# Kernel tuning notes

Hardware: AMD Instinct MI355X
Metric: run time of the kernel (lower is better)

The kernel has to match this reference:

```python
import jax, jax.numpy as jnp
import numpy as np

# ---- config ----
N = 500000
C = 32            # output_coordinate_dim
RES = [256, 256, 256, 64]
J = 2             # wavelet levels
BOUNDS = 1.3
# plane i -> (H, W) of stored plane, and (q, r) coord indices into [x,y,z,t]
# grid_sample convention: coord0 indexes W, coord1 indexes H
PLANE_RES = [(256, 256), (256, 256), (256, 64), (256, 256), (256, 64), (256, 64)]
COORD_IDX = [(0, 1), (0, 2), (3, 0), (1, 2), (3, 1), (3, 2)]

# coif4 decomposition low-pass filter (pywt), 24 taps
DEC_LO = np.array([
    -1.7849850030882614e-06, -3.2596802368833675e-06, 3.1229875865345646e-05,
    6.233903446100713e-05, -0.00025997455248771324, -0.0005890207562443383,
    0.0012665619292989445, 0.003751436157278457, -0.00565828668661072,
    -0.015211731527946259, 0.025082261844864097, 0.03933442712333749,
    -0.09622044203398798, -0.06662747426342504, 0.4343860564914685,
    0.782238930920499, 0.41530840703043026, -0.05607731331675481,
    -0.08126669968087875, 0.026682300156053072, 0.016068943964776348,
    -0.0073461663276420935, -0.0016294920126017326, 0.0008923136685823146],
    dtype=np.float32)
REC_LO = DEC_LO[::-1].copy()                                    # synthesis low-pass
REC_HI = (DEC_LO * ((-1.0) ** np.arange(DEC_LO.shape[0]))).astype(np.float32)  # QMF high-pass


def _up2(x, axis):
    """Insert zeros between samples along axis (upsample by 2)."""
    x = jnp.moveaxis(x, axis, -1)
    z = jnp.zeros(x.shape[:-1] + (2 * x.shape[-1],), x.dtype)
    z = z.at[..., ::2].set(x)
    return jnp.moveaxis(z, -1, axis)


def _circ_conv(x, f, axis):
    """Circular convolution along axis with a short fixed filter (periodization mode)."""
    out = f[0] * x
    for k in range(1, len(f)):
        out = out + f[k] * jnp.roll(x, k, axis=axis)
    return out


def _sfb1d(lo, hi, axis):
    """1D synthesis filter bank: upsample, filter, add. Length L -> 2L."""
    return _circ_conv(_up2(lo, axis), REC_LO, axis) + _circ_conv(_up2(hi, axis), REC_HI, axis)


def _sfb_level(ll, yh):
    """One inverse-DWT level. ll: [1,C,h,w], yh: [1,C,3,h,w] -> [1,C,2h,2w]."""
    lh, hl, hh = yh[:, :, 0], yh[:, :, 1], yh[:, :, 2]
    lo = _sfb1d(ll, lh, axis=2)   # combine along H
    hi = _sfb1d(hl, hh, axis=2)
    return _sfb1d(lo, hi, axis=3)  # combine along W


def _idwt2(yl, yhb, yha):
    """2-level inverse DWT (coif4, periodization). yl coarsest, yhb coarse detail, yha fine detail."""
    x = _sfb_level(yl, yhb)   # H/4 -> H/2
    x = _sfb_level(x, yha)    # H/2 -> H
    return x                  # [1, C, H, W]


def _bilinear_sample(plane, coords):
    """torch.grid_sample(bilinear, align_corners=True) equivalent.
    plane: [C,H,W]; coords: [N,2] in [-1,1], coords[:,0]->W, coords[:,1]->H. Returns [N,C]."""
    Cc, H, W = plane.shape
    x = jnp.clip((coords[:, 0] + 1.0) * 0.5 * (W - 1), 0.0, W - 1.0)
    y = jnp.clip((coords[:, 1] + 1.0) * 0.5 * (H - 1), 0.0, H - 1.0)
    x0 = jnp.clip(jnp.floor(x), 0.0, W - 2.0)
    y0 = jnp.clip(jnp.floor(y), 0.0, H - 2.0)
    wx = x - x0
    wy = y - y0
    x0i = x0.astype(jnp.int32); x1i = x0i + 1
    y0i = y0.astype(jnp.int32); y1i = y0i + 1
    v = (plane[:, y0i, x0i] * (1 - wy) * (1 - wx)
         + plane[:, y0i, x1i] * (1 - wy) * wx
         + plane[:, y1i, x0i] * wy * (1 - wx)
         + plane[:, y1i, x1i] * wy * wx)  # [C,N]
    return v.T


def setup_inputs() -> dict:
    key = jax.random.key(0)
    keys = jax.random.split(key, 2 + 6 * 3)
    inp = {}
    inp["pts"] = jax.random.uniform(keys[0], (N, 3), jnp.float32, -BOUNDS, BOUNDS)
    inp["timestamps"] = jax.random.uniform(keys[1], (N, 1), jnp.float32, 0.0, 1.0)
    for i, (H, W) in enumerate(PLANE_RES):
        k0, k1, k2 = keys[2 + 3 * i], keys[2 + 3 * i + 1], keys[2 + 3 * i + 2]
        # wavelet-domain learned parameters: yl coarsest approx, yha fine detail, yhb coarse detail
        inp[f"yl{i}"] = 0.3 + 0.1 * jax.random.normal(k0, (1, C, H // 4, W // 4), jnp.float32)
        inp[f"yha{i}"] = 0.05 * jax.random.normal(k1, (1, C, 3, H // 2, W // 2), jnp.float32)
        inp[f"yhb{i}"] = 0.05 * jax.random.normal(k2, (1, C, 3, H // 4, W // 4), jnp.float32)
    return inp


def reference(pts, timestamps,
              yl0, yha0, yhb0, yl1, yha1, yhb1, yl2, yha2, yhb2,
              yl3, yha3, yhb3, yl4, yha4, yhb4, yl5, yha5, yhb5):
    coefs = [(yl0, yha0, yhb0), (yl1, yha1, yhb1), (yl2, yha2, yhb2),
             (yl3, yha3, yhb3), (yl4, yha4, yhb4), (yl5, yha5, yhb5)]
    # normalize_aabb with aabb = [[B,B,B],[-B,-B,-B]]
    pts_n = (pts - BOUNDS) * (2.0 / (-2.0 * BOUNDS)) - 1.0
    t = timestamps * 2.0 - 1.0
    p4 = jnp.concatenate([pts_n, t], axis=-1)  # [N,4] = (x,y,z,t) in [-1,1]
    interp = jnp.ones((), jnp.float32)
    for (yl, yha, yhb), (q, r) in zip(coefs, COORD_IDX):
        plane = _idwt2(yl, yhb, yha)[0]                      # [C,H,W] IDWT reconstruction
        coords = jnp.stack([p4[:, q], p4[:, r]], axis=-1)    # [N,2]
        feat = _bilinear_sample(plane, coords)               # [N,C] gather
        interp = interp * feat                               # multiplicative fusion
    return interp
```

## Files before the change

### kernel.cpp

```cpp
#include <hip/hip_runtime.h>
#include <hip/hip_fp16.h>

#define NBIN 4096
#define NREP 8
#define SCAP 32
#define OVCAP 65536
#define BPB 4

__device__ __constant__ float DEC_LO[24] = {
    -1.7849850030882614e-06f, -3.2596802368833675e-06f, 3.1229875865345646e-05f,
    6.233903446100713e-05f, -0.00025997455248771324f, -0.0005890207562443383f,
    0.0012665619292989445f, 0.003751436157278457f, -0.00565828668661072f,
    -0.015211731527946259f, 0.025082261844864097f, 0.03933442712333749f,
    -0.09622044203398798f, -0.06662747426342504f, 0.4343860564914685f,
    0.782238930920499f, 0.41530840703043026f, -0.05607731331675481f,
    -0.08126669968087875f, 0.026682300156053072f, 0.016068943964776348f,
    -0.0073461663276420935f, -0.0016294920126017326f, 0.0008923136685823146f
};

struct PK {
    const float* yl[6];
    const float* yhb[6];
    const float* yha[6];
    float* x1[6];
    __half* lo2[6];
    __half* hi2[6];
    __half* planeH[6];
    const float* pts;
    const float* ts;
    int* cnt;
    int* cum;
    float4* binP4;
    int* binIdx;
    float4* ovP4;
    int* ovIdx;
    int Npts;
};

__device__ __forceinline__ void compute_p4(const float* pts, const float* ts, int p, float* p4) {
    const float sc = (float)(2.0 / (-2.0 * 1.3));
    p4[0] = (pts[p * 3 + 0] - 1.3f) * sc - 1.0f;
    p4[1] = (pts[p * 3 + 1] - 1.3f) * sc - 1.0f;
    p4[2] = (pts[p * 3 + 2] - 1.3f) * sc - 1.0f;
    p4[3] = ts[p] * 2.0f - 1.0f;
}

__device__ __forceinline__ int morton_key(const float* p4) {
    int key = 0;
#pragma unroll
    for (int d = 0; d < 4; ++d) {
        float u = (p4[d] + 1.0f) * 0.5f * 8.0f;
        int ci = (int)u;
        ci = ci < 0 ? 0 : (ci > 7 ? 7 : ci);
#pragma unroll
        for (int b = 0; b < 3; ++b) key |= ((ci >> b) & 1) << (b * 4 + d);
    }
    return key;
}

__global__ __launch_bounds__(256) void k1_l1_zero(PK a) {
    __shared__ struct { float lo[32 * 64], hi[32 * 64]; } sm;
    int bid = blockIdx.x, tid = threadIdx.x;

    if (bid < 768) {
        int rg = bid & 3, c = (bid >> 2) & 31, i = bid >> 7;
        int w4 = (i == 0 || i == 1 || i == 3) ? 64 : 16;
        int lw4 = (w4 == 64) ? 6 : 4;

        const float* llc = a.yl[i] + (size_t)c * 64 * w4;
        const float* lhc = a.yhb[i] + (size_t)(c * 3 + 0) * 64 * w4;
        const float* hlc = a.yhb[i] + (size_t)(c * 3 + 1) * 64 * w4;
        const float* hhc = a.yhb[i] + (size_t)(c * 3 + 2) * 64 * w4;

        for (int idx = tid; idx < (16 << lw4); idx += 256) {
            int mp = idx >> lw4, x = idx & (w4 - 1);
            int m = rg * 16 + mp;
            float lo0 = 0.f, lo1 = 0.f, hi0 = 0.f, hi1 = 0.f;
#pragma unroll
            for (int j = 0; j < 12; ++j) {
                int r = (m - j) & 63;
                int ii = (r << lw4) + x;
                float vll = llc[ii], vlh = lhc[ii], vhl = hlc[ii], vhh = hhc[ii];
                float rl0 = DEC_LO[23 - 2 * j], rl1 = DEC_LO[22 - 2 * j];
                float rh0 = DEC_LO[2 * j],      rh1 = -DEC_LO[2 * j + 1];
                lo0 += rl0 * vll + rh0 * vlh;
                lo1 += rl1 * vll + rh1 * vlh;
                hi0 += rl0 * vhl + rh0 * vhh;
                hi1 += rl1 * vhl + rh1 * vhh;
            }
            sm.lo[((2 * mp) << lw4) + x] = lo0;
            sm.lo[((2 * mp + 1) << lw4) + x] = lo1;
            sm.hi[((2 * mp) << lw4) + x] = hi0;
            sm.hi[((2 * mp + 1) << lw4) + x] = hi1;
        }
        __syncthreads();

        int w2 = w4 * 2;
        float* x1p = a.x1[i] + (size_t)c * 128 * w2;
        for (int idx = tid; idx < (32 << lw4); idx += 256) {
            int yl = idx >> lw4, mcol = idx & (w4 - 1);
            float o0 = 0.f, o1 = 0.f;
#pragma unroll
            for (int j = 0; j < 12; ++j) {
                int r = (mcol - j) & (w4 - 1);
                float vl = sm.lo[(yl << lw4) + r], vh = sm.hi[(yl << lw4) + r];
                o0 += DEC_LO[23 - 2 * j] * vl + DEC_LO[2 * j] * vh;
                o1 += DEC_LO[22 - 2 * j] * vl - DEC_LO[2 * j + 1] * vh;
            }
            *(float2*)(x1p + (size_t)(rg * 32 + yl) * w2 + 2 * mcol) = make_float2(o0, o1);
        }
    } else {
        int idx = (bid - 768) * 256 + tid;
        if (idx <= NREP * NBIN) a.cnt[idx] = 0;
    }
}

__global__ __launch_bounds__(256) void k2_v2_scatter(PK a) {
    int bid = blockIdx.x, tid = threadIdx.x;

    if (bid < 512) {
        const int S = 512 * 256;
        int rep = bid & 7;
        int t = bid * 256 + tid;
        for (int base = 0; base < a.Npts; base += 4 * S) {
            float4 q[4];
            int key[4], pi[4], pos[4];
#pragma unroll
            for (int k = 0; k < 4; ++k) {
                int p = base + t + k * S;
                pi[k] = p;
                if (p < a.Npts) {
                    float p4[4];
                    compute_p4(a.pts, a.ts, p, p4);
                    key[k] = morton_key(p4);
                    q[k] = make_float4(p4[0], p4[1], p4[2], p4[3]);
                } else {
                    key[k] = -1;
                }
            }
#pragma unroll
            for (int k = 0; k < 4; ++k)
                if (key[k] >= 0) pos[k] = atomicAdd(&a.cnt[rep * NBIN + key[k]], 1);
#pragma unroll
            for (int k = 0; k < 4; ++k) {
                if (key[k] < 0) continue;
                if (pos[k] < SCAP) {
                    size_t slot = ((size_t)rep * NBIN + key[k]) * SCAP + pos[k];
                    a.binP4[slot] = q[k];
                    a.binIdx[slot] = pi[k];
                } else {
                    int ov = atomicAdd(&a.cnt[NREP * NBIN], 1);
                    if (ov < OVCAP) {
                        a.ovP4[ov] = q[k];
                        a.ovIdx[ov] = pi[k];
                    }
                }
            }
        }
    } else {
        int ib = bid - 512;
        ib = (ib & 7) * 240 + (ib >> 3);

        const int boff[7] = {0, 512, 1024, 1152, 1664, 1792, 1920};
        int i = 0;
        while (i < 5 && ib >= boff[i + 1]) ++i;
        int lw2 = (i == 0 || i == 1 || i == 3) ? 7 : 5;
        int w2 = 1 << lw2;
        unsigned t = (unsigned)(ib - boff[i]) * 256u + tid;
        unsigned tpc = 32u << lw2;
        unsigned c = t >> (5 + lw2);
        unsigned rem = t & (tpc - 1);
        unsigned m = rem >> (lw2 - 2);
        unsigned x = (rem & (unsigned)((w2 >> 2) - 1)) * 4;
        unsigned hw = 128u << lw2;

        const float* llc = a.x1[i] + (size_t)c * hw;
        const float* lhc = a.yha[i] + (size_t)(c * 3 + 0) * hw;
        const float* hlc = a.yha[i] + (size_t)(c * 3 + 1) * hw;
        const float* hhc = a.yha[i] + (size_t)(c * 3 + 2) * hw;

        float4 acl0 = {0,0,0,0}, acl1 = {0,0,0,0}, ach0 = {0,0,0,0}, ach1 = {0,0,0,0};
#pragma unroll
        for (int j = 0; j < 12; ++j) {
            int r = ((int)m - j) & 127;
            unsigned idx = ((unsigned)r << lw2) + x;
            float4 vll = *(const float4*)(llc + idx);
            float4 vlh = *(const float4*)(lhc + idx);
            float4 vhl = *(const float4*)(hlc + idx);
            float4 vhh = *(const float4*)(hhc + idx);
            float rl0 = DEC_LO[23 - 2 * j], rl1 = DEC_LO[22 - 2 * j];
            float rh0 = DEC_LO[2 * j],      rh1 = -DEC_LO[2 * j + 1];
            acl0.x += rl0 * vll.x + rh0 * vlh.x;  acl0.y += rl0 * vll.y + rh0 * vlh.y;
            acl0.z += rl0 * vll.z + rh0 * vlh.z;  acl0.w += rl0 * vll.w + rh0 * vlh.w;
            acl1.x += rl1 * vll.x + rh1 * vlh.x;  acl1.y += rl1 * vll.y + rh1 * vlh.y;
            acl1.z += rl1 * vll.z + rh1 * vlh.z;  acl1.w += rl1 * vll.w + rh1 * vlh.w;
            ach0.x += rl0 * vhl.x + rh0 * vhh.x;  ach0.y += rl0 * vhl.y + rh0 * vhh.y;
            ach0.z += rl0 * vhl.z + rh0 * vhh.z;  ach0.w += rl0 * vhl.w + rh0 * vhh.w;
            ach1.x += rl1 * vhl.x + rh1 * vhh.x;  ach1.y += rl1 * vhl.y + rh1 * vhh.y;
            ach1.z += rl1 * vhl.z + rh1 * vhh.z;  ach1.w += rl1 * vhl.w + rh1 * vhh.w;
        }
        size_t ob = ((size_t)c * 256 + 2 * m) * w2 + x;
        __half* lp = a.lo2[i] + ob;
        *(__half2*)(lp)          = __floats2half2_rn(acl0.x, acl0.y);
        *(__half2*)(lp + 2)      = __floats2half2_rn(acl0.z, acl0.w);
        *(__half2*)(lp + w2)     = __floats2half2_rn(acl1.x, acl1.y);
        *(__half2*)(lp + w2 + 2) = __floats2half2_rn(acl1.z, acl1.w);
        __half* hpp = a.hi2[i] + ob;
        *(__half2*)(hpp)          = __floats2half2_rn(ach0.x, ach0.y);
        *(__half2*)(hpp + 2)      = __floats2half2_rn(ach0.z, ach0.w);
        *(__half2*)(hpp + w2)     = __floats2half2_rn(ach1.x, ach1.y);
        *(__half2*)(hpp + w2 + 2) = __floats2half2_rn(ach1.z, ach1.w);
    }
}

__global__ __launch_bounds__(256) void k3_ht(PK a) {
    __shared__ struct { __half lo[32 * 130], hi[32 * 130]; } sm;
    int bid = blockIdx.x, tid = threadIdx.x;

    if (bid < 1536) {
        int i = bid >> 8, y = bid & 255;
        int lw2 = (i == 0 || i == 1 || i == 3) ? 7 : 5;
        int w2 = 1 << lw2;
        int stride = w2 + 2;

        for (int idx = tid; idx < (32 << lw2); idx += 256) {
            int c = idx >> lw2, x = idx & (w2 - 1);
            size_t g = ((size_t)c * 256 + y) * w2 + x;
            sm.lo[c * stride + x] = a.lo2[i][g];
            sm.hi[c * stride + x] = a.hi2[i][g];
        }
        __syncthreads();

        int W = 2 * w2;
        __half* orow = a.planeH[i] + (size_t)y * W * 32;
        for (int idx = tid; idx < (32 << lw2); idx += 256) {
            int m = idx >> 5, c = idx & 31;
            float o0 = 0.f, o1 = 0.f;
#pragma unroll
            for (int j = 0; j < 12; ++j) {
                int r2 = m - j; if (r2 < 0) r2 += w2;
                float vl = __half2float(sm.lo[c * stride + r2]);
                float vh = __half2float(sm.hi[c * stride + r2]);
                o0 += DEC_LO[23 - 2 * j] * vl + DEC_LO[2 * j] * vh;
                o1 += DEC_LO[22 - 2 * j] * vl - DEC_LO[2 * j + 1] * vh;
            }
            orow[(2 * m) * 32 + c] = __float2half(o0);
            orow[(2 * m + 1) * 32 + c] = __float2half(o1);
        }
    } else {
        int bin = (bid - 1536) * 256 + tid;
        int c = 0;
#pragma unroll
        for (int r = 0; r < NREP; ++r) {
            int v = a.cnt[r * NBIN + bin];
            c += (v < SCAP ? v : SCAP);
            a.cum[bin * 8 + r] = c;
        }
    }
}

union H8 { float4 f4; __half h[8]; };

struct SK {
    const __half* pl[6];
    const float4* binP4;
    const int* binIdx;
    const int* cnt;
    const int* cum;
    const float4* ovP4;
    const int* ovIdx;
    float* out;
};

__device__ __forceinline__ void sample_pair(const SK& a,
        const float* p4A, int oA, int chA,
        const float* p4B, int oB, int chB, bool hasB) {
    const int PW[6] = {256, 256, 64, 256, 64, 64};
    const int QI[6] = {0, 0, 3, 1, 3, 3};
    const int RI[6] = {1, 2, 0, 2, 1, 2};
    float accA[8] = {1.f, 1.f, 1.f, 1.f, 1.f, 1.f, 1.f, 1.f};
    float accB[8] = {1.f, 1.f, 1.f, 1.f, 1.f, 1.f, 1.f, 1.f};
#pragma unroll
    for (int i = 0; i < 6; ++i) {
        int W = PW[i];
        float fxA = fminf(fmaxf((p4A[QI[i]] + 1.0f) * 0.5f * (float)(W - 1), 0.0f), (float)(W - 1));
        float fyA = fminf(fmaxf((p4A[RI[i]] + 1.0f) * 0.5f * 255.0f, 0.0f), 255.0f);
        float x0A = fminf(floorf(fxA), (float)(W - 2));
        float y0A = fminf(floorf(fyA), 254.0f);
        float wxA = fxA - x0A, wyA = fyA - y0A;
        const __half* baseA = a.pl[i] + ((size_t)(int)y0A * W + (int)x0A) * 32 + chA;
        float fxB = fminf(fmaxf((p4B[QI[i]] + 1.0f) * 0.5f * (float)(W - 1), 0.0f), (float)(W - 1));
        float fyB = fminf(fmaxf((p4B[RI[i]] + 1.0f) * 0.5f * 255.0f, 0.0f), 255.0f);
        float x0B = fminf(floorf(fxB), (float)(W - 2));
        float y0B = fminf(floorf(fyB), 254.0f);
        float wxB = fxB - x0B, wyB = fyB - y0B;
        const __half* baseB = a.pl[i] + ((size_t)(int)y0B * W + (int)x0B) * 32 + chB;

        H8 a00, a01, a10, a11, b00, b01, b10, b11;
        a00.f4 = *(const float4*)(baseA);
        a01.f4 = *(const float4*)(baseA + 32);
        a10.f4 = *(const float4*)(baseA + (size_t)W * 32);
        a11.f4 = *(const float4*)(baseA + (size_t)W * 32 + 32);
        b00.f4 = *(const float4*)(baseB);
        b01.f4 = *(const float4*)(baseB + 32);
        b10.f4 = *(const float4*)(baseB + (size_t)W * 32);
        b11.f4 = *(const float4*)(baseB + (size_t)W * 32 + 32);

        float wA00 = (1.f - wyA) * (1.f - wxA), wA01 = (1.f - wyA) * wxA;
        float wA10 = wyA * (1.f - wxA), wA11 = wyA * wxA;
        float wB00 = (1.f - wyB) * (1.f - wxB), wB01 = (1.f - wyB) * wxB;
        float wB10 = wyB * (1.f - wxB), wB11 = wyB * wxB;
#pragma unroll
        for (int k = 0; k < 8; ++k) {
            accA[k] *= wA00 * __half2float(a00.h[k]) + wA01 * __half2float(a01.h[k]) +
                       wA10 * __half2float(a10.h[k]) + wA11 * __half2float(a11.h[k]);
            accB[k] *= wB00 * __half2float(b00.h[k]) + wB01 * __half2float(b01.h[k]) +
                       wB10 * __half2float(b10.h[k]) + wB11 * __half2float(b11.h[k]);
        }
    }
    float* opA = a.out + (size_t)oA * 32 + chA;
    *(float4*)(opA)     = make_float4(accA[0], accA[1], accA[2], accA[3]);
    *(float4*)(opA + 4) = make_float4(accA[4], accA[5], accA[6], accA[7]);
    if (hasB) {
        float* opB = a.out + (size_t)oB * 32 + chB;
        *(float4*)(opB)     = make_float4(accB[0], accB[1], accB[2], accB[3]);
        *(float4*)(opB + 4) = make_float4(accB[4], accB[5], accB[6], accB[7]);
    }
}

__global__ __launch_bounds__(256) void k4_sample(SK a) {
    int bid = blockIdx.x, tid = threadIdx.x;
    if (bid < NBIN / BPB) {
        int xcd = bid & 7, g = bid >> 3;
        int binBase = xcd * (NBIN / 8) + g * BPB;

#pragma unroll
        for (int bb = 0; bb < BPB; ++bb) {
            int bin = binBase + bb;
            int4 u0 = *(const int4*)(a.cum + bin * 8);
            int4 u1 = *(const int4*)(a.cum + bin * 8 + 4);
            int cums[8] = {u0.x, u0.y, u0.z, u0.w, u1.x, u1.y, u1.z, u1.w};
            int n4 = cums[7] * 4;

            for (int l0 = tid; l0 < n4; l0 += 512) {
                int l1 = l0 + 256;
                bool hasB = l1 < n4;
                int lB = hasB ? l1 : l0;

                int sA = l0 >> 2, chA = (l0 & 3) << 3;
                int sB = lB >> 2, chB = (lB & 3) << 3;
                int rA = 0, bsA = 0, rB = 0, bsB = 0;
#pragma unroll
                for (int rr = 0; rr < NREP - 1; ++rr) {
                    if (sA >= cums[rr]) { rA = rr + 1; bsA = cums[rr]; }
                    if (sB >= cums[rr]) { rB = rr + 1; bsB = cums[rr]; }
                }
                size_t slotA = ((size_t)rA * NBIN + bin) * SCAP + (sA - bsA);
                size_t slotB = ((size_t)rB * NBIN + bin) * SCAP + (sB - bsB);
                float4 qA = a.binP4[slotA];
                float4 qB = a.binP4[slotB];
                int oA = a.binIdx[slotA];
                int oB = a.binIdx[slotB];
                float p4A[4] = {qA.x, qA.y, qA.z, qA.w};
                float p4B[4] = {qB.x, qB.y, qB.z, qB.w};
                sample_pair(a, p4A, oA, chA, p4B, oB, chB, hasB);
            }
        }
    } else {
        int ov = a.cnt[NREP * NBIN];
        ov = ov < OVCAP ? ov : OVCAP;
        int ov4 = ov * 4;
        for (int l0 = (bid - NBIN / BPB) * 256 + tid; l0 < ov4; l0 += 4096) {
            int l1 = l0 + 2048;
            bool hasB = l1 < ov4;
            int lB = hasB ? l1 : l0;
            int sA = l0 >> 2, chA = (l0 & 3) << 3;
            int sB = lB >> 2, chB = (lB & 3) << 3;
            float4 qA = a.ovP4[sA];
            float4 qB = a.ovP4[sB];
            float p4A[4] = {qA.x, qA.y, qA.z, qA.w};
            float p4B[4] = {qB.x, qB.y, qB.z, qB.w};
            sample_pair(a, p4A, a.ovIdx[sA], chA, p4B, a.ovIdx[sB], chB, hasB);
        }
    }
}

extern "C" void kernel_launch(void* const* d_in, const int* in_sizes, int n_in,
                              void* d_out, int out_size, void* d_ws, size_t ws_size,
                              hipStream_t stream) {
    const int PWt[6] = {256, 256, 64, 256, 64, 64};
    const int Npts = in_sizes[0] / 3;

    char* ws = (char*)d_ws;
    PK a;
    size_t off = 0;
    for (int i = 0; i < 6; ++i) {
        int W = PWt[i], w2 = W / 2;
        a.x1[i] = (float*)(ws + off);      off += (size_t)32 * 128 * w2 * 4;
        a.lo2[i] = (__half*)(ws + off);    off += (size_t)32 * 256 * w2 * 2;
        a.hi2[i] = (__half*)(ws + off);    off += (size_t)32 * 256 * w2 * 2;
        a.planeH[i] = (__half*)(ws + off); off += (size_t)256 * W * 32 * 2;
    }
    off = (off + 15) & ~(size_t)15;
    a.binP4 = (float4*)(ws + off);  off += (size_t)NREP * NBIN * SCAP * 16;
    a.ovP4 = (float4*)(ws + off);   off += (size_t)OVCAP * 16;
    a.binIdx = (int*)(ws + off);    off += (size_t)NREP * NBIN * SCAP * 4;
    a.ovIdx = (int*)(ws + off);     off += (size_t)OVCAP * 4;
    a.cnt = (int*)(ws + off);       off += ((size_t)NREP * NBIN + 1) * 4;
    off = (off + 15) & ~(size_t)15;
    a.cum = (int*)(ws + off);       off += (size_t)NBIN * 8 * 4;

    a.pts = (const float*)d_in[0];
    a.ts = (const float*)d_in[1];
    for (int i = 0; i < 6; ++i) {
        a.yl[i] = (const float*)d_in[2 + 3 * i];
        a.yha[i] = (const float*)d_in[3 + 3 * i];
        a.yhb[i] = (const float*)d_in[4 + 3 * i];
    }
    a.Npts = Npts;

    k1_l1_zero<<<768 + 129, 256, 0, stream>>>(a);
    k2_v2_scatter<<<512 + 1920, 256, 0, stream>>>(a);
    k3_ht<<<1536 + 16, 256, 0, stream>>>(a);

    SK s;
    for (int i = 0; i < 6; ++i) s.pl[i] = a.planeH[i];
    s.binP4 = a.binP4; s.binIdx = a.binIdx; s.cnt = a.cnt; s.cum = a.cum;
    s.ovP4 = a.ovP4; s.ovIdx = a.ovIdx;
    s.out = (float*)d_out;
    k4_sample<<<NBIN / BPB + 8, 256, 0, stream>>>(s);
}
```

Before: 249.7 us.

## Split planes into two 16-channel halves and map channel halves to XCDs

Stores each reconstructed plane as two channel-half planes ([2][H][W][16]) instead of interleaved 32 channels. The sampling kernel then assigns each block a single channel half and a bin subset, chosen by the low bits of the block id, so each XCD's L2 only caches one half-plane and a spatial slice of the bins. Each thread processes one point at a time instead of pairs, which cuts per-XCD cache footprint and register pressure. The cost is twice as many blocks and less memory-level parallelism per thread.

```diff
diff --git a/kernel.cpp b/kernel.cpp
--- a/kernel.cpp
+++ b/kernel.cpp
@@ -5,7 +5,6 @@
 #define NREP 8
 #define SCAP 32
 #define OVCAP 65536
-#define BPB 4
 
 __device__ __constant__ float DEC_LO[24] = {
     -1.7849850030882614e-06f, -3.2596802368833675e-06f, 3.1229875865345646e-05f,
@@ -232,7 +231,6 @@
         __syncthreads();
 
         int W = 2 * w2;
-        __half* orow = a.planeH[i] + (size_t)y * W * 32;
         for (int idx = tid; idx < (32 << lw2); idx += 256) {
             int m = idx >> 5, c = idx & 31;
             float o0 = 0.f, o1 = 0.f;
@@ -244,8 +242,10 @@
                 o0 += DEC_LO[23 - 2 * j] * vl + DEC_LO[2 * j] * vh;
                 o1 += DEC_LO[22 - 2 * j] * vl - DEC_LO[2 * j + 1] * vh;
             }
-            orow[(2 * m) * 32 + c] = __float2half(o0);
-            orow[(2 * m + 1) * 32 + c] = __float2half(o1);
+            size_t off = (size_t)(c >> 4) * 256 * W * 16
+                       + ((size_t)y * W + 2 * m) * 16 + (c & 15);
+            a.planeH[i][off] = __float2half(o0);
+            a.planeH[i][off + 16] = __float2half(o1);
         }
     } else {
         int bin = (bid - 1536) * 256 + tid;
@@ -272,115 +272,82 @@
     float* out;
 };
 
-__device__ __forceinline__ void sample_pair(const SK& a,
-        const float* p4A, int oA, int chA,
-        const float* p4B, int oB, int chB, bool hasB) {
+__device__ __forceinline__ void sample8p(const SK& a, const float* p4, int oidx, int c2, int sub) {
     const int PW[6] = {256, 256, 64, 256, 64, 64};
     const int QI[6] = {0, 0, 3, 1, 3, 3};
     const int RI[6] = {1, 2, 0, 2, 1, 2};
-    float accA[8] = {1.f, 1.f, 1.f, 1.f, 1.f, 1.f, 1.f, 1.f};
-    float accB[8] = {1.f, 1.f, 1.f, 1.f, 1.f, 1.f, 1.f, 1.f};
+    float acc[8] = {1.f, 1.f, 1.f, 1.f, 1.f, 1.f, 1.f, 1.f};
 #pragma unroll
     for (int i = 0; i < 6; ++i) {
         int W = PW[i];
-        float fxA = fminf(fmaxf((p4A[QI[i]] + 1.0f) * 0.5f * (float)(W - 1), 0.0f), (float)(W - 1));
-        float fyA = fminf(fmaxf((p4A[RI[i]] + 1.0f) * 0.5f * 255.0f, 0.0f), 255.0f);
-        float x0A = fminf(floorf(fxA), (float)(W - 2));
-        float y0A = fminf(floorf(fyA), 254.0f);
-        float wxA = fxA - x0A, wyA = fyA - y0A;
-        const __half* baseA = a.pl[i] + ((size_t)(int)y0A * W + (int)x0A) * 32 + chA;
-        float fxB = fminf(fmaxf((p4B[QI[i]] + 1.0f) * 0.5f * (float)(W - 1), 0.0f), (float)(W - 1));
-        float fyB = fminf(fmaxf((p4B[RI[i]] + 1.0f) * 0.5f * 255.0f, 0.0f), 255.0f);
-        float x0B = fminf(floorf(fxB), (float)(W - 2));
-        float y0B = fminf(floorf(fyB), 254.0f);
-        float wxB = fxB - x0B, wyB = fyB - y0B;
-        const __half* baseB = a.pl[i] + ((size_t)(int)y0B * W + (int)x0B) * 32 + chB;
-
-        H8 a00, a01, a10, a11, b00, b01, b10, b11;
-        a00.f4 = *(const float4*)(baseA);
-        a01.f4 = *(const float4*)(baseA + 32);
-        a10.f4 = *(const float4*)(baseA + (size_t)W * 32);
-        a11.f4 = *(const float4*)(baseA + (size_t)W * 32 + 32);
-        b00.f4 = *(const float4*)(baseB);
-        b01.f4 = *(const float4*)(baseB + 32);
-        b10.f4 = *(const float4*)(baseB + (size_t)W * 32);
-        b11.f4 = *(const float4*)(baseB + (size_t)W * 32 + 32);
-
-        float wA00 = (1.f - wyA) * (1.f - wxA), wA01 = (1.f - wyA) * wxA;
-        float wA10 = wyA * (1.f - wxA), wA11 = wyA * wxA;
-        float wB00 = (1.f - wyB) * (1.f - wxB), wB01 = (1.f - wyB) * wxB;
-        float wB10 = wyB * (1.f - wxB), wB11 = wyB * wxB;
+        float fx = fminf(fmaxf((p4[QI[i]] + 1.0f) * 0.5f * (float)(W - 1), 0.0f), (float)(W - 1));
+        float fy = fminf(fmaxf((p4[RI[i]] + 1.0f) * 0.5f * 255.0f, 0.0f), 255.0f);
+        float x0 = fminf(floorf(fx), (float)(W - 2));
+        float y0 = fminf(floorf(fy), 254.0f);
+        float wx = fx - x0, wy = fy - y0;
+        int xi = (int)x0, yi = (int)y0;
+
+        const __half* base = a.pl[i] + ((((size_t)c2 * 256 + yi) * W + xi) << 4) + sub * 8;
+        H8 u00, u01, u10, u11;
+        u00.f4 = *(const float4*)(base);
+        u01.f4 = *(const float4*)(base + 16);
+        u10.f4 = *(const float4*)(base + (size_t)W * 16);
+        u11.f4 = *(const float4*)(base + (size_t)W * 16 + 16);
+
+        float w00 = (1.f - wy) * (1.f - wx), w01 = (1.f - wy) * wx;
+        float w10 = wy * (1.f - wx), w11 = wy * wx;
 #pragma unroll
         for (int k = 0; k < 8; ++k) {
-            accA[k] *= wA00 * __half2float(a00.h[k]) + wA01 * __half2float(a01.h[k]) +
-                       wA10 * __half2float(a10.h[k]) + wA11 * __half2float(a11.h[k]);
-            accB[k] *= wB00 * __half2float(b00.h[k]) + wB01 * __half2float(b01.h[k]) +
-                       wB10 * __half2float(b10.h[k]) + wB11 * __half2float(b11.h[k]);
-        }
-    }
-    float* opA = a.out + (size_t)oA * 32 + chA;
-    *(float4*)(opA)     = make_float4(accA[0], accA[1], accA[2], accA[3]);
-    *(float4*)(opA + 4) = make_float4(accA[4], accA[5], accA[6], accA[7]);
-    if (hasB) {
-        float* opB = a.out + (size_t)oB * 32 + chB;
-        *(float4*)(opB)     = make_float4(accB[0], accB[1], accB[2], accB[3]);
-        *(float4*)(opB + 4) = make_float4(accB[4], accB[5], accB[6], accB[7]);
-    }
+            float f = w00 * __half2float(u00.h[k]) + w01 * __half2float(u01.h[k]) +
+                      w10 * __half2float(u10.h[k]) + w11 * __half2float(u11.h[k]);
+            acc[k] *= f;
+        }
+    }
+    float* op = a.out + (size_t)oidx * 32 + c2 * 16 + sub * 8;
+    *(float4*)(op) = make_float4(acc[0], acc[1], acc[2], acc[3]);
+    *(float4*)(op + 4) = make_float4(acc[4], acc[5], acc[6], acc[7]);
 }
 
 __global__ __launch_bounds__(256) void k4_sample(SK a) {
     int bid = blockIdx.x, tid = threadIdx.x;
-    if (bid < NBIN / BPB) {
-        int xcd = bid & 7, g = bid >> 3;
-        int binBase = xcd * (NBIN / 8) + g * BPB;
-
-#pragma unroll
-        for (int bb = 0; bb < BPB; ++bb) {
-            int bin = binBase + bb;
+    if (bid < 2048) {
+        int g7 = bid & 7;
+        int c2 = g7 >> 2, yh = (g7 >> 1) & 1, zh = g7 & 1;
+        int g = bid >> 3;
+
+#pragma unroll
+        for (int pr = 0; pr < 2; ++pr) {
+            int myj = g * 4 + 2 * pr + (tid >= 128 ? 1 : 0);
+            int bin = ((myj >> 9) << 11) | (zh << 10) | (yh << 9) | (myj & 511);
+
             int4 u0 = *(const int4*)(a.cum + bin * 8);
             int4 u1 = *(const int4*)(a.cum + bin * 8 + 4);
             int cums[8] = {u0.x, u0.y, u0.z, u0.w, u1.x, u1.y, u1.z, u1.w};
-            int n4 = cums[7] * 4;
-
-            for (int l0 = tid; l0 < n4; l0 += 512) {
-                int l1 = l0 + 256;
-                bool hasB = l1 < n4;
-                int lB = hasB ? l1 : l0;
-
-                int sA = l0 >> 2, chA = (l0 & 3) << 3;
-                int sB = lB >> 2, chB = (lB & 3) << 3;
-                int rA = 0, bsA = 0, rB = 0, bsB = 0;
-#pragma unroll
-                for (int rr = 0; rr < NREP - 1; ++rr) {
-                    if (sA >= cums[rr]) { rA = rr + 1; bsA = cums[rr]; }
-                    if (sB >= cums[rr]) { rB = rr + 1; bsB = cums[rr]; }
-                }
-                size_t slotA = ((size_t)rA * NBIN + bin) * SCAP + (sA - bsA);
-                size_t slotB = ((size_t)rB * NBIN + bin) * SCAP + (sB - bsB);
-                float4 qA = a.binP4[slotA];
-                float4 qB = a.binP4[slotB];
-                int oA = a.binIdx[slotA];
-                int oB = a.binIdx[slotB];
-                float p4A[4] = {qA.x, qA.y, qA.z, qA.w};
-                float p4B[4] = {qB.x, qB.y, qB.z, qB.w};
-                sample_pair(a, p4A, oA, chA, p4B, oB, chB, hasB);
+            int n = cums[7];
+
+            int lp = tid & 127;
+            int s = lp >> 1, sub = lp & 1;
+            for (; s < n; s += 64) {
+                int r = 0, bs = 0;
+#pragma unroll
+                for (int rr = 0; rr < NREP - 1; ++rr)
+                    if (s >= cums[rr]) { r = rr + 1; bs = cums[rr]; }
+                size_t slot = ((size_t)r * NBIN + bin) * SCAP + (s - bs);
+                float4 q = a.binP4[slot];
+                int o = a.binIdx[slot];
+                float p4[4] = {q.x, q.y, q.z, q.w};
+                sample8p(a, p4, o, c2, sub);
             }
         }
     } else {
         int ov = a.cnt[NREP * NBIN];
         ov = ov < OVCAP ? ov : OVCAP;
         int ov4 = ov * 4;
-        for (int l0 = (bid - NBIN / BPB) * 256 + tid; l0 < ov4; l0 += 4096) {
-            int l1 = l0 + 2048;
-            bool hasB = l1 < ov4;
-            int lB = hasB ? l1 : l0;
-            int sA = l0 >> 2, chA = (l0 & 3) << 3;
-            int sB = lB >> 2, chB = (lB & 3) << 3;
-            float4 qA = a.ovP4[sA];
-            float4 qB = a.ovP4[sB];
-            float p4A[4] = {qA.x, qA.y, qA.z, qA.w};
-            float p4B[4] = {qB.x, qB.y, qB.z, qB.w};
-            sample_pair(a, p4A, a.ovIdx[sA], chA, p4B, a.ovIdx[sB], chB, hasB);
+        for (int l0 = (bid - 2048) * 256 + tid; l0 < ov4; l0 += 8 * 256) {
+            int s = l0 >> 2, c2 = (l0 >> 1) & 1, sub = l0 & 1;
+            float4 q = a.ovP4[s];
+            float p4[4] = {q.x, q.y, q.z, q.w};
+            sample8p(a, p4, a.ovIdx[s], c2, sub);
         }
     }
 }
@@ -428,5 +395,5 @@
     s.binP4 = a.binP4; s.binIdx = a.binIdx; s.cnt = a.cnt; s.cum = a.cum;
     s.ovP4 = a.ovP4; s.ovIdx = a.ovIdx;
     s.out = (float*)d_out;
-    k4_sample<<<NBIN / BPB + 8, 256, 0, stream>>>(s);
-}
+    k4_sample<<<2048 + 8, 256, 0, stream>>>(s);
+}
```

Result: slower. 264.7 us (+6.0%).
